# Optimization experiments

Measured on AMD Instinct MI355X. Metric: run time of the kernel, lower is better.

## Reference

```python
import jax, jax.numpy as jnp
import numpy as np

HEADS = 8
DIM_HEAD = 64
SCALE = DIM_HEAD ** -0.5


def setup_inputs() -> dict:
    key = jax.random.key(0)
    ks = jax.random.split(key, 5)
    B, N, M, D = 8, 1024, 1024, 512
    inner = HEADS * DIM_HEAD  # 512
    return {
        "x": jax.random.normal(ks[0], (B, N, D), dtype=jnp.float32),
        "context": jax.random.normal(ks[1], (B, M, D), dtype=jnp.float32),
        "Wq": jax.random.normal(ks[2], (D, inner), dtype=jnp.float32) * (D ** -0.5),
        "Wkv": jax.random.normal(ks[3], (D, 2 * inner), dtype=jnp.float32) * (D ** -0.5),
        "Wo": jax.random.normal(ks[4], (inner, D), dtype=jnp.float32) * (inner ** -0.5),
        "bo": jnp.zeros((D,), dtype=jnp.float32),
    }


def reference(x, context, Wq, Wkv, Wo, bo):
    B, N, D = x.shape
    M = context.shape[1]
    q = x @ Wq                      # [B, N, inner]
    kv = context @ Wkv              # [B, M, 2*inner]
    k, v = jnp.split(kv, 2, axis=-1)
    # b n (h d) -> b h n d
    split_heads = lambda t: t.reshape(t.shape[0], t.shape[1], HEADS, DIM_HEAD).transpose(0, 2, 1, 3)
    q, k, v = split_heads(q), split_heads(k), split_heads(v)
    dots = jnp.einsum('bhid,bhjd->bhij', q, k) * SCALE  # [B, H, N, M]
    attn = jax.nn.softmax(dots, axis=-1)
    out = jnp.einsum('bhij,bhjd->bhid', attn, v)        # [B, H, N, d]
    out = out.transpose(0, 2, 1, 3).reshape(B, N, HEADS * DIM_HEAD)
    return out @ Wo + bo            # [B, N, D]
```

## Files before the change

### kernel.cpp

```cpp
#include <hip/hip_runtime.h>
#include <stdint.h>

#define LOG2E 1.44269504088896340736f
#define QSCALE (0.125f * LOG2E)

typedef __bf16 bf16x8 __attribute__((ext_vector_type(8)));
typedef float floatx4 __attribute__((ext_vector_type(4)));

__device__ __forceinline__ unsigned short bfbits(float f) {
  __bf16 h = (__bf16)f;
  return __builtin_bit_cast(unsigned short, h);
}

__device__ __forceinline__ float fast_exp2(float x) {
#if __has_builtin(__builtin_amdgcn_exp2f)
  return __builtin_amdgcn_exp2f(x);
#else
  return exp2f(x);
#endif
}

__device__ __forceinline__ void gl2lds16(const void* g, void* l) {
  __builtin_amdgcn_global_load_lds((const __attribute__((address_space(1))) void*)g,
                                   (__attribute__((address_space(3))) void*)l, 16, 0, 0);
}

__global__ __launch_bounds__(256)
void prep_kernel(const float* __restrict__ x, const float* __restrict__ ctx,
                 const float* __restrict__ Wq, const float* __restrict__ Wkv,
                 const float* __restrict__ Wo,
                 unsigned short* __restrict__ Xb, unsigned short* __restrict__ Cb,
                 unsigned short* __restrict__ WqT, unsigned short* __restrict__ WkvT,
                 unsigned short* __restrict__ WoT) {
  int blk = blockIdx.x;
  int tid = threadIdx.x;
  if (blk < 8192) {
    const float* in = blk < 4096 ? x : ctx;
    unsigned short* out = blk < 4096 ? Xb : Cb;
    int i = (((blk & 4095) * 256) + tid) * 4;
    float4 v = *(const float4*)(in + i);
    unsigned long long pk = (unsigned long long)bfbits(v.x)
                          | ((unsigned long long)bfbits(v.y) << 16)
                          | ((unsigned long long)bfbits(v.z) << 32)
                          | ((unsigned long long)bfbits(v.w) << 48);
    *(unsigned long long*)(out + i) = pk;
  } else {
    __shared__ float tile[32][33];
    int t = blk - 8192;
    const float* in; unsigned short* out; int N; int tb;
    if (t < 256)      { in = Wq;  out = WqT;  N = 512;  tb = t; }
    else if (t < 768) { in = Wkv; out = WkvT; N = 1024; tb = t - 256; }
    else              { in = Wo;  out = WoT;  N = 512;  tb = t - 768; }
    const int K = 512;
    int nbx = N / 32;
    int n0 = (tb % nbx) * 32, k0 = (tb / nbx) * 32;
    int tx = tid & 31, ty = tid >> 5;
#pragma unroll
    for (int r = ty; r < 32; r += 8)
      tile[r][tx] = in[(long)(k0 + r) * N + n0 + tx];
    __syncthreads();
#pragma unroll
    for (int r = ty; r < 32; r += 8)
      out[(long)(n0 + r) * K + k0 + tx] = bfbits(tile[tx][r]);
  }
}

__global__ __launch_bounds__(256)
void proj_gemm(const unsigned short* __restrict__ Xb, const unsigned short* __restrict__ Cb,
               const unsigned short* __restrict__ WqT, const unsigned short* __restrict__ WkvT,
               unsigned short* __restrict__ Qb, unsigned short* __restrict__ Kb,
               unsigned short* __restrict__ Vt) {
  __shared__ unsigned short As[2][128 * 32];
  __shared__ unsigned short Bs[2][128 * 32];

  int idx0 = blockIdx.x;
  int idx = (idx0 & 7) * 96 + (idx0 >> 3);
  const unsigned short* A; const unsigned short* Bt;
  long bm, bn; int role;
  if (idx < 256) { role = 0; A = Xb; Bt = WqT;  bn = (long)(idx & 3) * 128; bm = (long)(idx >> 2) * 128; }
  else { int j = idx - 256; role = 1; A = Cb; Bt = WkvT; bn = (long)(j & 7) * 128; bm = (long)(j >> 3) * 128; }

  const int tid = threadIdx.x;
  const int wave = tid >> 6;
  const int lane = tid & 63;
  const int l15 = lane & 15;
  const int q4 = lane >> 4;
  const int wm = (wave & 1) * 64;
  const int wn = (wave >> 1) * 64;
  const int K = 512;

  int aoff[2], boff[2], lds16[2];
#pragma unroll
  for (int cc = 0; cc < 2; ++cc) {
    int c = cc * 256 + tid;
    int r = c >> 2, kc = c & 3;
    int gc = kc ^ ((r >> 1) & 3);
    aoff[cc] = (int)(bm + r) * K + gc * 8;
    boff[cc] = (int)(bn + r) * K + gc * 8;
    lds16[cc] = c * 16;
  }
  const int csw = (q4 ^ ((l15 >> 1) & 3)) * 8;
  int arow[4], brow[4];
#pragma unroll
  for (int i = 0; i < 4; ++i) {
    arow[i] = (wm + i * 16 + l15) * 32 + csw;
    brow[i] = (wn + i * 16 + l15) * 32 + csw;
  }

  floatx4 acc[4][4];
#pragma unroll
  for (int i = 0; i < 4; ++i)
#pragma unroll
    for (int j = 0; j < 4; ++j) { acc[i][j][0]=0.f; acc[i][j][1]=0.f; acc[i][j][2]=0.f; acc[i][j][3]=0.f; }

#define PROJ_STAGE(BUF, KOFF)                                              \
  {                                                                        \
    _Pragma("unroll")                                                      \
    for (int cc = 0; cc < 2; ++cc) {                                       \
      gl2lds16(A + aoff[cc] + (KOFF), (char*)As[(BUF)] + lds16[cc]);       \
      gl2lds16(Bt + boff[cc] + (KOFF), (char*)Bs[(BUF)] + lds16[cc]);      \
    }                                                                      \
  }

#define PROJ_STEP(T, CUR, DO_STAGE)                                        \
  {                                                                        \
    if (DO_STAGE) PROJ_STAGE((CUR) ^ 1, ((T) + 1) * 32);                   \
    bf16x8 af[4], bfr[4];                                                  \
    _Pragma("unroll")                                                      \
    for (int i = 0; i < 4; ++i) af[i] = *(const bf16x8*)(As[(CUR)] + arow[i]); \
    _Pragma("unroll")                                                      \
    for (int j = 0; j < 4; ++j) bfr[j] = *(const bf16x8*)(Bs[(CUR)] + brow[j]); \
    _Pragma("unroll")                                                      \
    for (int i = 0; i < 4; ++i)                                            \
      _Pragma("unroll")                                                    \
      for (int j = 0; j < 4; ++j)                                          \
        acc[i][j] = __builtin_amdgcn_mfma_f32_16x16x32_bf16(af[i], bfr[j], acc[i][j], 0, 0, 0); \
    if ((T) < 15) __syncthreads();                                         \
  }

  PROJ_STAGE(0, 0);
  __syncthreads();
  for (int tt = 0; tt < 8; ++tt) {
    PROJ_STEP(2 * tt, 0, true);
    PROJ_STEP(2 * tt + 1, 1, (tt < 7));
  }
#undef PROJ_STEP
#undef PROJ_STAGE

  const bool vrole = (role == 1) && (bn >= 512);
#pragma unroll
  for (int i = 0; i < 4; ++i) {
#pragma unroll
    for (int j = 0; j < 4; ++j) {
      long col = bn + wn + j * 16 + l15;
      if (vrole) {
        long h = (col - 512) >> 6, d = col & 63;
        long row0 = bm + wm + i * 16 + q4 * 4;
        long b = row0 >> 10, m0 = row0 & 1023;
        unsigned long long pk = (unsigned long long)bfbits(acc[i][j][0])
                              | ((unsigned long long)bfbits(acc[i][j][1]) << 16)
                              | ((unsigned long long)bfbits(acc[i][j][2]) << 32)
                              | ((unsigned long long)bfbits(acc[i][j][3]) << 48);
        *(unsigned long long*)(Vt + ((b * 8 + h) * 64 + d) * 1024 + m0) = pk;
      } else {
        long h = col >> 6, d = col & 63;
#pragma unroll
        for (int r = 0; r < 4; ++r) {
          long row = bm + wm + i * 16 + q4 * 4 + r;
          long b = row >> 10, n = row & 1023;
          float v = acc[i][j][r];
          if (role == 0) Qb[((b * 8 + h) * 1024 + n) * 64 + d] = bfbits(v * QSCALE);
          else           Kb[((b * 8 + h) * 1024 + n) * 64 + d] = bfbits(v);
        }
      }
    }
  }
}

__global__ __launch_bounds__(512)
void attn_kernel(const unsigned short* __restrict__ Qb,
                 const unsigned short* __restrict__ Kb,
                 const unsigned short* __restrict__ Vt,
                 unsigned short* __restrict__ Ob)
{
  __shared__ unsigned short Ksm[2][4096];
  __shared__ unsigned short Vsm[2][4096];
  __shared__ unsigned short Psm[128 * 64];

  const int tid = threadIdx.x;
  const int wave = tid >> 6;
  const int lane = tid & 63;
  const int l15 = lane & 15;
  const int q4 = lane >> 4;
  const int bid = blockIdx.x;
  const int lin = (bid & 7) * 64 + (bid >> 3);
  const int bh = lin >> 3;
  const int nb = lin & 7;

  const long qrow0 = (long)bh * 1024 + nb * 128 + wave * 16;

  bf16x8 qf[2];
#pragma unroll
  for (int ks = 0; ks < 2; ++ks)
    qf[ks] = *(const bf16x8*)(Qb + (qrow0 + l15) * 64 + ks * 32 + q4 * 8);

  floatx4 acc[4];
#pragma unroll
  for (int d = 0; d < 4; ++d) { acc[d][0]=0.f; acc[d][1]=0.f; acc[d][2]=0.f; acc[d][3]=0.f; }
  float suml = 0.0f;

  const unsigned short* Kbase = Kb + (long)bh * 65536;
  const unsigned short* Vbase = Vt + (long)bh * 65536;
  const int jrow = tid >> 3;
  const int cact = (tid & 7) ^ (jrow & 7);
  const int koff = jrow * 64 + cact * 8;
  const int voff = jrow * 1024 + cact * 8;
  const int myl = tid * 16;

  const int s7 = l15 & 7;
  int kfo[2][4];
  int pao[2];
  int pwo[4];
#pragma unroll
  for (int ks = 0; ks < 2; ++ks) {
#pragma unroll
    for (int jn = 0; jn < 4; ++jn)
      kfo[ks][jn] = (jn * 16 + l15) * 64 + (((ks * 4 + q4) ^ s7) * 8);
    pao[ks] = (wave * 16 + l15) * 64 + (((ks * 4 + q4) ^ s7) * 8);
  }
#pragma unroll
  for (int jn = 0; jn < 4; ++jn)
    pwo[jn] = (wave * 16 + l15) * 64 + (((jn * 2 + (q4 >> 1)) ^ s7) * 8) + (q4 & 1) * 4;

  gl2lds16(Kbase + koff, (char*)Ksm[0] + myl);
  gl2lds16(Vbase + voff, (char*)Vsm[0] + myl);

#define ATTN_TILE(TIDX, CUR, STAGE)                                                          \
  {                                                                                          \
    __syncthreads();                                                                         \
    if (STAGE) {                                                                             \
      gl2lds16(Kbase + ((TIDX) + 1) * 4096 + koff, (char*)Ksm[(CUR) ^ 1] + myl);             \
      gl2lds16(Vbase + ((TIDX) + 1) * 64 + voff, (char*)Vsm[(CUR) ^ 1] + myl);               \
    }                                                                                        \
    floatx4 st[4];                                                                           \
    _Pragma("unroll")                                                                        \
    for (int jn = 0; jn < 4; ++jn) {                                                         \
      st[jn][0] = 0.f; st[jn][1] = 0.f; st[jn][2] = 0.f; st[jn][3] = 0.f;                    \
    }                                                                                        \
    _Pragma("unroll")                                                                        \
    for (int ks = 0; ks < 2; ++ks) {                                                         \
      bf16x8 kfr[4];                                                                         \
      _Pragma("unroll")                                                                      \
      for (int jn = 0; jn < 4; ++jn)                                                         \
        kfr[jn] = *(const bf16x8*)(Ksm[(CUR)] + kfo[ks][jn]);                                \
      __builtin_amdgcn_s_setprio(1);                                                         \
      _Pragma("unroll")                                                                      \
      for (int jn = 0; jn < 4; ++jn)                                                         \
        st[jn] = __builtin_amdgcn_mfma_f32_16x16x32_bf16(kfr[jn], qf[ks], st[jn], 0, 0, 0);  \
      __builtin_amdgcn_s_setprio(0);                                                         \
    }                                                                                        \
    bf16x8 vbt[2][4];        \
    _Pragma("unroll")                                                                        \
    for (int ks = 0; ks < 2; ++ks)                                                           \
      _Pragma("unroll")                                                                      \
      for (int dn = 0; dn < 4; ++dn)                                                         \
        vbt[ks][dn] = *(const bf16x8*)(Vsm[(CUR)] + kfo[ks][dn]);                            \
    _Pragma("unroll")                                                                        \
    for (int jn = 0; jn < 4; ++jn) {                                                         \
      float p0 = fast_exp2(st[jn][0]);                                                       \
      float p1 = fast_exp2(st[jn][1]);                                                       \
      float p2 = fast_exp2(st[jn][2]);                                                       \
      float p3 = fast_exp2(st[jn][3]);                                                       \
      suml += (p0 + p1) + (p2 + p3);                                                         \
      unsigned int lo = (unsigned int)bfbits(p0) | ((unsigned int)bfbits(p1) << 16);         \
      unsigned int hi = (unsigned int)bfbits(p2) | ((unsigned int)bfbits(p3) << 16);         \
      unsigned long long pk = (unsigned long long)lo | ((unsigned long long)hi << 32);       \
      *(unsigned long long*)(Psm + pwo[jn]) = pk;                                            \
    }                                                                                        \
    __asm__ volatile("s_waitcnt lgkmcnt(0)" ::: "memory");                                   \
    _Pragma("unroll")                                                                        \
    for (int ks = 0; ks < 2; ++ks) {                                                         \
      bf16x8 pa = *(const bf16x8*)(Psm + pao[ks]);                                           \
      __builtin_amdgcn_s_setprio(1);                                                         \
      _Pragma("unroll")                                                                      \
      for (int dn = 0; dn < 4; ++dn)                                                         \
        acc[dn] = __builtin_amdgcn_mfma_f32_16x16x32_bf16(pa, vbt[ks][dn], acc[dn], 0, 0, 0);\
      __builtin_amdgcn_s_setprio(0);                                                         \
    }                                                                                        \
  }

  for (int tt = 0; tt < 8; ++tt) {
    ATTN_TILE(2 * tt, 0, true);
    ATTN_TILE(2 * tt + 1, 1, (tt < 7));
  }
#undef ATTN_TILE

  float l = suml;
  l += __shfl_xor(l, 16, 64);
  l += __shfl_xor(l, 32, 64);
  float inv = 1.0f / l;
  float invr[4];
#pragma unroll
  for (int r = 0; r < 4; ++r) invr[r] = __shfl(inv, q4 * 4 + r, 64);

  const int b = bh >> 3, h = bh & 7;
#pragma unroll
  for (int dn = 0; dn < 4; ++dn) {
#pragma unroll
    for (int r = 0; r < 4; ++r) {
      long row = (long)b * 1024 + nb * 128 + wave * 16 + q4 * 4 + r;
      long col = h * 64 + dn * 16 + l15;
      Ob[row * 512 + col] = bfbits(acc[dn][r] * invr[r]);
    }
  }
}

__global__ __launch_bounds__(256)
void out_gemm(const unsigned short* __restrict__ A,
              const unsigned short* __restrict__ Bt,
              float* __restrict__ outF, const float* __restrict__ bias) {
  __shared__ unsigned short As[2][64 * 32];
  __shared__ unsigned short Bs[2][64 * 32];

  int bid = blockIdx.x;
  int swz = (bid & 7) * 128 + (bid >> 3);
  const long bm = (long)(swz >> 3) * 64;
  const long bn = (long)(swz & 7) * 64;

  const int tid = threadIdx.x;
  const int wave = tid >> 6;
  const int lane = tid & 63;
  const int l15 = lane & 15;
  const int q4 = lane >> 4;
  const int wm = (wave & 1) * 32;
  const int wn = (wave >> 1) * 32;
  const int K = 512, N = 512;

  const int r = tid >> 2, kc = tid & 3;
  const int gc = kc ^ ((r >> 1) & 3);
  const int aoff = (int)(bm + r) * K + gc * 8;
  const int boff = (int)(bn + r) * K + gc * 8;
  const int myl = tid * 16;

  const int csw = (q4 ^ ((l15 >> 1) & 3)) * 8;
  int arow[2], brow[2];
#pragma unroll
  for (int i = 0; i < 2; ++i) {
    arow[i] = (wm + i * 16 + l15) * 32 + csw;
    brow[i] = (wn + i * 16 + l15) * 32 + csw;
  }

  floatx4 acc[2][2];
#pragma unroll
  for (int i = 0; i < 2; ++i)
#pragma unroll
    for (int j = 0; j < 2; ++j) { acc[i][j][0]=0.f; acc[i][j][1]=0.f; acc[i][j][2]=0.f; acc[i][j][3]=0.f; }

#define OUT_STAGE(BUF, KOFF)                                        \
  {                                                                 \
    gl2lds16(A + aoff + (KOFF), (char*)As[(BUF)] + myl);            \
    gl2lds16(Bt + boff + (KOFF), (char*)Bs[(BUF)] + myl);           \
  }

#define OUT_STEP(T, CUR, DO_STAGE)                                  \
  {                                                                 \
    if (DO_STAGE) OUT_STAGE((CUR) ^ 1, ((T) + 1) * 32);             \
    bf16x8 af[2], bfr[2];                                           \
    _Pragma("unroll")                                               \
    for (int i = 0; i < 2; ++i) af[i] = *(const bf16x8*)(As[(CUR)] + arow[i]); \
    _Pragma("unroll")                                               \
    for (int j = 0; j < 2; ++j) bfr[j] = *(const bf16x8*)(Bs[(CUR)] + brow[j]); \
    _Pragma("unroll")                                               \
    for (int i = 0; i < 2; ++i)                                     \
      _Pragma("unroll")                                             \
      for (int j = 0; j < 2; ++j)                                   \
        acc[i][j] = __builtin_amdgcn_mfma_f32_16x16x32_bf16(af[i], bfr[j], acc[i][j], 0, 0, 0); \
    if ((T) < 15) __syncthreads();                                  \
  }

  OUT_STAGE(0, 0);
  __syncthreads();
  for (int tt = 0; tt < 8; ++tt) {
    OUT_STEP(2 * tt, 0, true);
    OUT_STEP(2 * tt + 1, 1, (tt < 7));
  }
#undef OUT_STEP
#undef OUT_STAGE

#pragma unroll
  for (int i = 0; i < 2; ++i) {
#pragma unroll
    for (int j = 0; j < 2; ++j) {
      long col = bn + wn + j * 16 + l15;
      float bv = bias[col];
#pragma unroll
      for (int rr = 0; rr < 4; ++rr) {
        long row = bm + wm + i * 16 + q4 * 4 + rr;
        outF[row * (long)N + col] = acc[i][j][rr] + bv;
      }
    }
  }
}

extern "C" void kernel_launch(void* const* d_in, const int* in_sizes, int n_in,
                              void* d_out, int out_size, void* d_ws, size_t ws_size,
                              hipStream_t stream) {
  const float* x   = (const float*)d_in[0];
  const float* ctx = (const float*)d_in[1];
  const float* Wq  = (const float*)d_in[2];
  const float* Wkv = (const float*)d_in[3];
  const float* Wo  = (const float*)d_in[4];
  const float* bo  = (const float*)d_in[5];
  float* out = (float*)d_out;

  char* ws = (char*)d_ws;
  unsigned short* Xb   = (unsigned short*)(ws);
  unsigned short* Cb   = (unsigned short*)(ws + (8u  << 20));
  unsigned short* WqT  = (unsigned short*)(ws + (16u << 20));
  unsigned short* WkvT = (unsigned short*)(ws + (17u << 20));
  unsigned short* WoT  = (unsigned short*)(ws + (19u << 20));
  unsigned short* Qb   = (unsigned short*)(ws + (20u << 20));
  unsigned short* Kb   = (unsigned short*)(ws + (28u << 20));
  unsigned short* Vt   = (unsigned short*)(ws + (36u << 20));
  unsigned short* Ob   = (unsigned short*)(ws + (44u << 20));

  prep_kernel<<<9216, 256, 0, stream>>>(x, ctx, Wq, Wkv, Wo, Xb, Cb, WqT, WkvT, WoT);
  proj_gemm<<<768, 256, 0, stream>>>(Xb, Cb, WqT, WkvT, Qb, Kb, Vt);
  attn_kernel<<<512, 512, 0, stream>>>(Qb, Kb, Vt, Ob);
  out_gemm<<<1024, 256, 0, stream>>>(Ob, WoT, out, bo);
}
```

Before: 158.1 us.

## Fuse fp32-to-bf16 conversion of x and context into projection GEMM A-load

Removes the separate prep pass that converted x and context to bf16 in workspace. The projection GEMM now loads fp32 A tiles into registers, converts them to bf16 and writes them swizzled into LDS after the MFMA step, while B still streams via direct global-to-LDS loads. This saves a full write and re-read of the bf16 activations. In exchange, A traffic per GEMM tile doubles in bytes, each tile is re-read by several column blocks, and register pressure rises from the staged float4 values.

```diff
diff --git a/kernel.cpp b/kernel.cpp
--- a/kernel.cpp
+++ b/kernel.cpp
@@ -26,47 +26,32 @@
 }
 
 __global__ __launch_bounds__(256)
-void prep_kernel(const float* __restrict__ x, const float* __restrict__ ctx,
-                 const float* __restrict__ Wq, const float* __restrict__ Wkv,
+void prep_kernel(const float* __restrict__ Wq, const float* __restrict__ Wkv,
                  const float* __restrict__ Wo,
-                 unsigned short* __restrict__ Xb, unsigned short* __restrict__ Cb,
                  unsigned short* __restrict__ WqT, unsigned short* __restrict__ WkvT,
                  unsigned short* __restrict__ WoT) {
-  int blk = blockIdx.x;
+  __shared__ float tile[32][33];
+  int t = blockIdx.x;
   int tid = threadIdx.x;
-  if (blk < 8192) {
-    const float* in = blk < 4096 ? x : ctx;
-    unsigned short* out = blk < 4096 ? Xb : Cb;
-    int i = (((blk & 4095) * 256) + tid) * 4;
-    float4 v = *(const float4*)(in + i);
-    unsigned long long pk = (unsigned long long)bfbits(v.x)
-                          | ((unsigned long long)bfbits(v.y) << 16)
-                          | ((unsigned long long)bfbits(v.z) << 32)
-                          | ((unsigned long long)bfbits(v.w) << 48);
-    *(unsigned long long*)(out + i) = pk;
-  } else {
-    __shared__ float tile[32][33];
-    int t = blk - 8192;
-    const float* in; unsigned short* out; int N; int tb;
-    if (t < 256)      { in = Wq;  out = WqT;  N = 512;  tb = t; }
-    else if (t < 768) { in = Wkv; out = WkvT; N = 1024; tb = t - 256; }
-    else              { in = Wo;  out = WoT;  N = 512;  tb = t - 768; }
-    const int K = 512;
-    int nbx = N / 32;
-    int n0 = (tb % nbx) * 32, k0 = (tb / nbx) * 32;
-    int tx = tid & 31, ty = tid >> 5;
-#pragma unroll
-    for (int r = ty; r < 32; r += 8)
-      tile[r][tx] = in[(long)(k0 + r) * N + n0 + tx];
-    __syncthreads();
-#pragma unroll
-    for (int r = ty; r < 32; r += 8)
-      out[(long)(n0 + r) * K + k0 + tx] = bfbits(tile[tx][r]);
-  }
+  const float* in; unsigned short* out; int N; int tb;
+  if (t < 256)      { in = Wq;  out = WqT;  N = 512;  tb = t; }
+  else if (t < 768) { in = Wkv; out = WkvT; N = 1024; tb = t - 256; }
+  else              { in = Wo;  out = WoT;  N = 512;  tb = t - 768; }
+  const int K = 512;
+  int nbx = N / 32;
+  int n0 = (tb % nbx) * 32, k0 = (tb / nbx) * 32;
+  int tx = tid & 31, ty = tid >> 5;
+#pragma unroll
+  for (int r = ty; r < 32; r += 8)
+    tile[r][tx] = in[(long)(k0 + r) * N + n0 + tx];
+  __syncthreads();
+#pragma unroll
+  for (int r = ty; r < 32; r += 8)
+    out[(long)(n0 + r) * K + k0 + tx] = bfbits(tile[tx][r]);
 }
 
 __global__ __launch_bounds__(256)
-void proj_gemm(const unsigned short* __restrict__ Xb, const unsigned short* __restrict__ Cb,
+void proj_gemm(const float* __restrict__ Xf, const float* __restrict__ Cf,
                const unsigned short* __restrict__ WqT, const unsigned short* __restrict__ WkvT,
                unsigned short* __restrict__ Qb, unsigned short* __restrict__ Kb,
                unsigned short* __restrict__ Vt) {
@@ -75,10 +60,10 @@
 
   int idx0 = blockIdx.x;
   int idx = (idx0 & 7) * 96 + (idx0 >> 3);
-  const unsigned short* A; const unsigned short* Bt;
+  const float* A; const unsigned short* Bt;
   long bm, bn; int role;
-  if (idx < 256) { role = 0; A = Xb; Bt = WqT;  bn = (long)(idx & 3) * 128; bm = (long)(idx >> 2) * 128; }
-  else { int j = idx - 256; role = 1; A = Cb; Bt = WkvT; bn = (long)(j & 7) * 128; bm = (long)(j >> 3) * 128; }
+  if (idx < 256) { role = 0; A = Xf; Bt = WqT;  bn = (long)(idx & 3) * 128; bm = (long)(idx >> 2) * 128; }
+  else { int j = idx - 256; role = 1; A = Cf; Bt = WkvT; bn = (long)(j & 7) * 128; bm = (long)(j >> 3) * 128; }
 
   const int tid = threadIdx.x;
   const int wave = tid >> 6;
@@ -89,15 +74,21 @@
   const int wn = (wave >> 1) * 64;
   const int K = 512;
 
-  int aoff[2], boff[2], lds16[2];
+  const int ars = tid >> 1, ahalf = tid & 1;
+  const long aF = (bm + ars) * 512 + ahalf * 16;
+  int awr[2];
+#pragma unroll
+  for (int w = 0; w < 2; ++w)
+    awr[w] = ars * 32 + (((ahalf * 2 + w) ^ ((ars >> 1) & 3)) * 8);
+
+  int boff[2], lds16b[2];
 #pragma unroll
   for (int cc = 0; cc < 2; ++cc) {
     int c = cc * 256 + tid;
     int r = c >> 2, kc = c & 3;
     int gc = kc ^ ((r >> 1) & 3);
-    aoff[cc] = (int)(bm + r) * K + gc * 8;
     boff[cc] = (int)(bn + r) * K + gc * 8;
-    lds16[cc] = c * 16;
+    lds16b[cc] = c * 16;
   }
   const int csw = (q4 ^ ((l15 >> 1) & 3)) * 8;
   int arow[4], brow[4];
@@ -113,18 +104,38 @@
 #pragma unroll
     for (int j = 0; j < 4; ++j) { acc[i][j][0]=0.f; acc[i][j][1]=0.f; acc[i][j][2]=0.f; acc[i][j][3]=0.f; }
 
-#define PROJ_STAGE(BUF, KOFF)                                              \
+  float4 va[4];
+
+#define PROJ_LOADA(KOFF)                                                   \
   {                                                                        \
     _Pragma("unroll")                                                      \
-    for (int cc = 0; cc < 2; ++cc) {                                       \
-      gl2lds16(A + aoff[cc] + (KOFF), (char*)As[(BUF)] + lds16[cc]);       \
-      gl2lds16(Bt + boff[cc] + (KOFF), (char*)Bs[(BUF)] + lds16[cc]);      \
+    for (int w = 0; w < 4; ++w)                                            \
+      va[w] = *(const float4*)(A + aF + (KOFF) + w * 4);                   \
+  }
+
+#define PROJ_WRITEA(BUF)                                                   \
+  {                                                                        \
+    _Pragma("unroll")                                                      \
+    for (int w = 0; w < 2; ++w) {                                          \
+      uint4 pk;                                                            \
+      pk.x = (unsigned)bfbits(va[2*w].x) | ((unsigned)bfbits(va[2*w].y) << 16);     \
+      pk.y = (unsigned)bfbits(va[2*w].z) | ((unsigned)bfbits(va[2*w].w) << 16);     \
+      pk.z = (unsigned)bfbits(va[2*w+1].x) | ((unsigned)bfbits(va[2*w+1].y) << 16); \
+      pk.w = (unsigned)bfbits(va[2*w+1].z) | ((unsigned)bfbits(va[2*w+1].w) << 16); \
+      *(uint4*)(As[(BUF)] + awr[w]) = pk;                                  \
     }                                                                      \
+  }
+
+#define PROJ_STAGEB(BUF, KOFF)                                             \
+  {                                                                        \
+    _Pragma("unroll")                                                      \
+    for (int cc = 0; cc < 2; ++cc)                                         \
+      gl2lds16(Bt + boff[cc] + (KOFF), (char*)Bs[(BUF)] + lds16b[cc]);     \
   }
 
 #define PROJ_STEP(T, CUR, DO_STAGE)                                        \
   {                                                                        \
-    if (DO_STAGE) PROJ_STAGE((CUR) ^ 1, ((T) + 1) * 32);                   \
+    if (DO_STAGE) { PROJ_LOADA(((T) + 1) * 32); PROJ_STAGEB((CUR) ^ 1, ((T) + 1) * 32); } \
     bf16x8 af[4], bfr[4];                                                  \
     _Pragma("unroll")                                                      \
     for (int i = 0; i < 4; ++i) af[i] = *(const bf16x8*)(As[(CUR)] + arow[i]); \
@@ -135,17 +146,22 @@
       _Pragma("unroll")                                                    \
       for (int j = 0; j < 4; ++j)                                          \
         acc[i][j] = __builtin_amdgcn_mfma_f32_16x16x32_bf16(af[i], bfr[j], acc[i][j], 0, 0, 0); \
+    if (DO_STAGE) PROJ_WRITEA((CUR) ^ 1);                                  \
     if ((T) < 15) __syncthreads();                                         \
   }
 
-  PROJ_STAGE(0, 0);
+  PROJ_LOADA(0);
+  PROJ_STAGEB(0, 0);
+  PROJ_WRITEA(0);
   __syncthreads();
   for (int tt = 0; tt < 8; ++tt) {
     PROJ_STEP(2 * tt, 0, true);
     PROJ_STEP(2 * tt + 1, 1, (tt < 7));
   }
 #undef PROJ_STEP
-#undef PROJ_STAGE
+#undef PROJ_STAGEB
+#undef PROJ_WRITEA
+#undef PROJ_LOADA
 
   const bool vrole = (role == 1) && (bn >= 512);
 #pragma unroll
@@ -414,8 +430,6 @@
   float* out = (float*)d_out;
 
   char* ws = (char*)d_ws;
-  unsigned short* Xb   = (unsigned short*)(ws);
-  unsigned short* Cb   = (unsigned short*)(ws + (8u  << 20));
   unsigned short* WqT  = (unsigned short*)(ws + (16u << 20));
   unsigned short* WkvT = (unsigned short*)(ws + (17u << 20));
   unsigned short* WoT  = (unsigned short*)(ws + (19u << 20));
@@ -424,8 +438,8 @@
   unsigned short* Vt   = (unsigned short*)(ws + (36u << 20));
   unsigned short* Ob   = (unsigned short*)(ws + (44u << 20));
 
-  prep_kernel<<<9216, 256, 0, stream>>>(x, ctx, Wq, Wkv, Wo, Xb, Cb, WqT, WkvT, WoT);
-  proj_gemm<<<768, 256, 0, stream>>>(Xb, Cb, WqT, WkvT, Qb, Kb, Vt);
+  prep_kernel<<<1024, 256, 0, stream>>>(Wq, Wkv, Wo, WqT, WkvT, WoT);
+  proj_gemm<<<768, 256, 0, stream>>>(x, ctx, WqT, WkvT, Qb, Kb, Vt);
   attn_kernel<<<512, 512, 0, stream>>>(Qb, Kb, Vt, Ob);
   out_gemm<<<1024, 256, 0, stream>>>(Ob, WoT, out, bo);
 }
```

Result: no change. 156.4 us (-1.1%).
